# Kernel optimization log

Measured on AMD Instinct MI355X. Metric: run time of the kernel, lower is better.

Reference implementation:

```python
import jax, jax.numpy as jnp
import numpy as np

D_MODEL = 1024
N_HEADS = 16
D_HEAD = D_MODEL // N_HEADS
ROPE_BASE = 10000.0


def setup_inputs() -> dict:
    key = jax.random.key(0)
    k1, k2, k3, k4, k5 = jax.random.split(key, 5)
    std = 0.02 / np.sqrt(2 * 12)  # scaled_xavier with n_layers=12
    x = jax.random.normal(k1, (2, 2048, D_MODEL), dtype=jnp.float32)
    qkv_w = jax.random.normal(k2, (3 * D_MODEL, D_MODEL), dtype=jnp.float32) * std
    qkv_b = jnp.zeros((3 * D_MODEL,), dtype=jnp.float32)
    proj_w = jax.random.normal(k3, (D_MODEL, D_MODEL), dtype=jnp.float32) * std
    proj_b = jnp.zeros((D_MODEL,), dtype=jnp.float32)
    return {"x": x, "qkv_w": qkv_w, "qkv_b": qkv_b, "proj_w": proj_w, "proj_b": proj_b}


def _rope_cos_sin(seq_len, dtype):
    inv_freq = 1.0 / (ROPE_BASE ** (jnp.arange(0, D_HEAD, 2, dtype=jnp.float32) / D_HEAD))
    t = jnp.arange(seq_len, dtype=jnp.float32)
    freqs = jnp.einsum("t,d->td", t, inv_freq)          # [S, Dh/2]
    freqs = jnp.concatenate([freqs, freqs], axis=-1)      # [S, Dh]
    return jnp.cos(freqs).astype(dtype), jnp.sin(freqs).astype(dtype)


def _rotate_half(x):
    x1, x2 = jnp.split(x, 2, axis=-1)
    return jnp.concatenate([-x2, x1], axis=-1)


def reference(x, qkv_w, qkv_b, proj_w, proj_b):
    B, S, D = x.shape
    H, Dh = N_HEADS, D_HEAD
    scale = 1.0 / np.sqrt(Dh)

    qkv = x @ qkv_w.T + qkv_b                              # [B, S, 3D]
    qkv = qkv.reshape(B, S, 3, H, Dh)
    q = jnp.transpose(qkv[:, :, 0], (0, 2, 1, 3))          # [B, H, S, Dh]
    k = jnp.transpose(qkv[:, :, 1], (0, 2, 1, 3))
    v = jnp.transpose(qkv[:, :, 2], (0, 2, 1, 3))

    cos, sin = _rope_cos_sin(S, x.dtype)                   # [S, Dh]
    q = q * cos + _rotate_half(q) * sin
    k = k * cos + _rotate_half(k) * sin

    scores = jnp.einsum("bhsd,bhtd->bhst", q, k) * scale   # [B, H, S, S]
    causal = jnp.triu(jnp.ones((S, S), dtype=bool), k=1)
    neg = jnp.finfo(scores.dtype).min
    scores = jnp.where(causal[None, None], neg, scores)

    probs = jax.nn.softmax(scores, axis=-1)
    ctx = jnp.einsum("bhst,bhtd->bhsd", probs, v)          # [B, H, S, Dh]
    out = jnp.transpose(ctx, (0, 2, 1, 3)).reshape(B, S, D)
    out = out @ proj_w.T + proj_b
    return out
```

## Files before the change

kernel.cpp:

```cpp
#include <hip/hip_runtime.h>
#include <hip/hip_bf16.h>

#define BATCH 2
#define SEQ   2048
#define DMODEL 1024
#define NHEADS 16
#define DHEAD  64
#define MTOT   (BATCH * SEQ)
#define QKSTR  2048

typedef __attribute__((ext_vector_type(8))) short bf16x8;
typedef __attribute__((ext_vector_type(4))) short bf16x4;
typedef __attribute__((ext_vector_type(4))) float f32x4;

__device__ __forceinline__ void glds16(const void* g, void* l)
{
    __builtin_amdgcn_global_load_lds(
        (const __attribute__((address_space(1))) unsigned int*)g,
        (__attribute__((address_space(3))) unsigned int*)l, 16, 0, 0);
}

__device__ __forceinline__ unsigned cvt_pk_bf16(float lo, float hi)
{
    unsigned r;
    asm("v_cvt_pk_bf16_f32 %0, %1, %2" : "=v"(r) : "v"(lo), "v"(hi));
    return r;
}

__global__ void cast_all_kernel(
    const float* __restrict__ a, __hip_bfloat16* __restrict__ oa, int na4,
    const float* __restrict__ b, __hip_bfloat16* __restrict__ ob, int nb4,
    const float* __restrict__ c, __hip_bfloat16* __restrict__ oc, int nc4)
{
    int i = blockIdx.x * blockDim.x + threadIdx.x;
    const float* src; __hip_bfloat16* dst; int j = i;
    if (j < na4) { src = a; dst = oa; }
    else {
        j -= na4;
        if (j < nb4) { src = b; dst = ob; }
        else {
            j -= nb4;
            if (j >= nc4) return;
            src = c; dst = oc;
        }
    }
    float4 v = ((const float4*)src)[j];
    __hip_bfloat16 tmp[4];
    tmp[0] = __float2bfloat16(v.x);
    tmp[1] = __float2bfloat16(v.y);
    tmp[2] = __float2bfloat16(v.z);
    tmp[3] = __float2bfloat16(v.w);
    *(uint2*)(dst + 4 * (size_t)j) = *(const uint2*)tmp;
}

#define GBK 64

__device__ __forceinline__ void store_out(float* p, float v) { *p = v; }
__device__ __forceinline__ void store_out(__hip_bfloat16* p, float v) { *p = __float2bfloat16(v); }

template <typename OutT, int MODE, int TM, int TN, int MINW>
__global__ __launch_bounds__(256, MINW) void gemm_bias_kernel(
    const __hip_bfloat16* __restrict__ A, const __hip_bfloat16* __restrict__ W,
    const float* __restrict__ bias, OutT* __restrict__ out,
    __hip_bfloat16* __restrict__ vtg,
    int M, int N, int K)
{
    const int MI = TM / 32;
    const int NI = TN / 32;
    const int bm = blockIdx.x * TM;
    const int bn = blockIdx.y * TN;
    const int tid = threadIdx.x;
    const int wave = tid >> 6;
    const int lane = tid & 63;
    const int quad = lane >> 4;
    const int l16 = lane & 15;
    const int wm = (wave & 1) * (TM / 2);
    const int wn = (wave >> 1) * (TN / 2);

    __shared__ __hip_bfloat16 As[TM * GBK];
    __shared__ __hip_bfloat16 Bs[TN * GBK];

    f32x4 acc[MI][NI] = {};

    const int srow = lane >> 3;
    const int gc8 = (((lane & 7) ^ srow)) * 8;

    for (int kt = 0; kt < K; kt += GBK) {
#pragma unroll
        for (int t = 0; t < MI; t++) {
            int i = wave * MI + t;
            glds16(A + (size_t)(bm + i * 8 + srow) * K + kt + gc8, As + i * 512);
        }
#pragma unroll
        for (int t = 0; t < NI; t++) {
            int i = wave * NI + t;
            glds16(W + (size_t)(bn + i * 8 + srow) * K + kt + gc8, Bs + i * 512);
        }
        __syncthreads();

#pragma unroll
        for (int kk = 0; kk < 2; kk++) {
            bf16x8 af[MI], bfr[NI];
#pragma unroll
            for (int i = 0; i < MI; i++) {
                int ra = wm + i * 16 + l16;
                af[i] = *(const bf16x8*)(As + ra * 64 + (((kk << 2) + quad) ^ (ra & 7)) * 8);
            }
#pragma unroll
            for (int i = 0; i < NI; i++) {
                int rb = wn + i * 16 + l16;
                bfr[i] = *(const bf16x8*)(Bs + rb * 64 + (((kk << 2) + quad) ^ (rb & 7)) * 8);
            }
#pragma unroll
            for (int mi = 0; mi < MI; mi++)
#pragma unroll
                for (int ni = 0; ni < NI; ni++)
                    acc[mi][ni] = __builtin_amdgcn_mfma_f32_16x16x32_bf16(
                        af[mi], bfr[ni], acc[mi][ni], 0, 0, 0);
        }
        __syncthreads();
    }

    if (MODE == 1 && (bn + wn) < 2 * DMODEL) {
#pragma unroll
        for (int ni = 0; ni < 2; ni++) {
            int col = bn + wn + ni * 16 + l16;
            int i32 = col & 31;
            float invf = exp2f(-13.287712379549449f * (float)i32 * (1.0f / 32.0f));
            float b1 = bias[col], b2 = bias[col + 32];
#pragma unroll
            for (int mi = 0; mi < MI; mi++) {
#pragma unroll
                for (int r = 0; r < 4; r++) {
                    int row = bm + wm + mi * 16 + quad * 4 + r;
                    int s = row & (SEQ - 1);
                    float ang = (float)s * invf;
                    float sn, cs;
                    __sincosf(ang, &sn, &cs);
                    float x1 = acc[mi][ni][r] + b1;
                    float x2 = acc[mi][ni + 2][r] + b2;
                    store_out(&out[(size_t)row * QKSTR + col], x1 * cs - x2 * sn);
                    store_out(&out[(size_t)row * QKSTR + col + 32], x2 * cs + x1 * sn);
                }
            }
        }
    } else if (MODE == 1) {
#pragma unroll
        for (int ni = 0; ni < NI; ni++) {
            int colg = bn + wn + ni * 16 + l16;
            int vcol = colg - 2 * DMODEL;
            int hh = vcol >> 6, dh = vcol & 63;
            float bv = bias[colg];
#pragma unroll
            for (int mi = 0; mi < MI; mi++) {
                int row0 = bm + wm + mi * 16 + quad * 4;
                int bb = row0 >> 11;
                int ss = row0 & (SEQ - 1);
                __hip_bfloat16 tmp[4];
#pragma unroll
                for (int r = 0; r < 4; r++)
                    tmp[r] = __float2bfloat16(acc[mi][ni][r] + bv);
                *(uint2*)(vtg + (((size_t)bb * NHEADS + hh) * DHEAD + dh) * SEQ + ss) =
                    *(uint2*)tmp;
            }
        }
    } else {
#pragma unroll
        for (int mi = 0; mi < MI; mi++)
#pragma unroll
            for (int ni = 0; ni < NI; ni++) {
                int col = bn + wn + ni * 16 + l16;
                float bv = bias[col];
#pragma unroll
                for (int r = 0; r < 4; r++) {
                    int row = bm + wm + mi * 16 + quad * 4 + r;
                    store_out(&out[(size_t)row * N + col], acc[mi][ni][r] + bv);
                }
            }
    }
}

__global__ __launch_bounds__(256, 5) void flash_attn_mfma_kernel(
    const __hip_bfloat16* __restrict__ qkb,
    const __hip_bfloat16* __restrict__ vtg,
    __hip_bfloat16* __restrict__ ctx)
{
    const int bh = blockIdx.x;
    const int b = bh >> 4, h = bh & 15;
    const int y = blockIdx.y;
    const int qt = (y < 8) ? 31 - y : (y < 16) ? y - 8 : (y < 24) ? 39 - y : y - 16;
    const int tid = threadIdx.x;
    const int w = tid >> 6;
    const int lane = tid & 63;
    const int quad = lane >> 4;
    const int l16 = lane & 15;

    __shared__ alignas(16) __hip_bfloat16 Ks[2][64 * 64];
    __shared__ alignas(16) __hip_bfloat16 Vt[2][64 * 64];

    const __hip_bfloat16* qbase = qkb + (size_t)b * SEQ * QKSTR + h * DHEAD;
    const __hip_bfloat16* kbase = qbase + DMODEL;
    const __hip_bfloat16* vbase = vtg + (size_t)bh * DHEAD * SEQ;

    const __hip_bfloat16* qrow = qbase + (size_t)(qt * 64 + w * 16 + l16) * QKSTR;
    bf16x8 qf0 = *(const bf16x8*)(qrow + quad * 8);
    bf16x8 qf1 = *(const bf16x8*)(qrow + 32 + quad * 8);

    const int srow = lane >> 3;
    const int gc8 = ((lane & 7) ^ srow) * 8;
    const __hip_bfloat16* kg = kbase + (size_t)(w * 16 + srow) * QKSTR + gc8;
    const __hip_bfloat16* vg = vbase + (size_t)(w * 16 + srow) * SEQ + gc8;

    const int xr = l16 & 7;
    const int fo0 = l16 * 64 + ((quad ^ xr) << 3);
    const int fo1 = l16 * 64 + (((4 + quad) ^ xr) << 3);
    int vbse[4], vchk[4];
#pragma unroll
    for (int dt = 0; dt < 4; dt++)
        vbse[dt] = (dt * 16 + l16) * 64 + (quad & 1) * 4;
#pragma unroll
    for (int nt = 0; nt < 4; nt++)
        vchk[nt] = (((nt << 1) + (quad >> 1)) ^ xr) << 3;

    const short ov = (l16 == 0) ? (short)0x3F80 : (short)0;
    const bf16x4 ones4 = {ov, ov, ov, ov};

    f32x4 oacc[5] = {};

    auto stage = [&](int t, int buf) {
        const __hip_bfloat16* kt_ = kg + (size_t)t * 64 * QKSTR;
        const __hip_bfloat16* vt_ = vg + t * 64;
        glds16(kt_,              &Ks[buf][w * 1024]);
        glds16(kt_ + 8 * QKSTR,  &Ks[buf][w * 1024 + 512]);
        glds16(vt_,              &Vt[buf][w * 1024]);
        glds16(vt_ + 8 * SEQ,    &Vt[buf][w * 1024 + 512]);
    };

    stage(0, 0);

    for (int jt = 0; jt <= qt; jt++) {
        __syncthreads();
        const int cur = jt & 1;
        if (jt < qt) stage(jt + 1, cur ^ 1);
        const __hip_bfloat16* ks = Ks[cur];
        const __hip_bfloat16* vs = Vt[cur];

        f32x4 s4[4] = {};
        __builtin_amdgcn_s_setprio(1);
#pragma unroll
        for (int nt = 0; nt < 4; nt++)
            s4[nt] = __builtin_amdgcn_mfma_f32_16x16x32_bf16(
                *(const bf16x8*)(ks + nt * 1024 + fo0), qf0, s4[nt], 0, 0, 0);
#pragma unroll
        for (int nt = 0; nt < 4; nt++)
            s4[nt] = __builtin_amdgcn_mfma_f32_16x16x32_bf16(
                *(const bf16x8*)(ks + nt * 1024 + fo1), qf1, s4[nt], 0, 0, 0);
        __builtin_amdgcn_s_setprio(0);

        const bool diag = (jt == qt);
        const int qq = w * 16 + l16;
#pragma unroll
        for (int nt = 0; nt < 4; nt++) {
            float p0 = exp2f(s4[nt][0] * 0.1803368801f);
            float p1 = exp2f(s4[nt][1] * 0.1803368801f);
            float p2 = exp2f(s4[nt][2] * 0.1803368801f);
            float p3 = exp2f(s4[nt][3] * 0.1803368801f);
            if (diag) {
                int k0 = nt * 16 + quad * 4;
                p0 = (k0 + 0 <= qq) ? p0 : 0.f;
                p1 = (k0 + 1 <= qq) ? p1 : 0.f;
                p2 = (k0 + 2 <= qq) ? p2 : 0.f;
                p3 = (k0 + 3 <= qq) ? p3 : 0.f;
            }
            union { unsigned u[2]; bf16x4 v; } pu;
            pu.u[0] = cvt_pk_bf16(p0, p1);
            pu.u[1] = cvt_pk_bf16(p2, p3);
            const bf16x4 pa = pu.v;

            __builtin_amdgcn_s_setprio(1);
#pragma unroll
            for (int dt = 0; dt < 4; dt++)
                oacc[dt] = __builtin_amdgcn_mfma_f32_16x16x16bf16_1k(
                    pa, *(const bf16x4*)(vs + vbse[dt] + vchk[nt]), oacc[dt], 0, 0, 0);
            oacc[4] = __builtin_amdgcn_mfma_f32_16x16x16bf16_1k(
                pa, ones4, oacc[4], 0, 0, 0);
            __builtin_amdgcn_s_setprio(0);
        }
    }

#pragma unroll
    for (int r = 0; r < 4; r++) {
        float lv = __shfl(oacc[4][r], lane & 48);
        float il = 1.0f / lv;
        int qg = qt * 64 + w * 16 + quad * 4 + r;
        __hip_bfloat16* op = ctx + (((size_t)b * SEQ + qg) * NHEADS + h) * DHEAD + l16;
#pragma unroll
        for (int dt = 0; dt < 4; dt++)
            op[dt * 16] = __float2bfloat16(oacc[dt][r] * il);
    }
}

extern "C" void kernel_launch(void* const* d_in, const int* in_sizes, int n_in,
                              void* d_out, int out_size, void* d_ws, size_t ws_size,
                              hipStream_t stream)
{
    const float* x      = (const float*)d_in[0];
    const float* qkv_w  = (const float*)d_in[1];
    const float* qkv_b  = (const float*)d_in[2];
    const float* proj_w = (const float*)d_in[3];
    const float* proj_b = (const float*)d_in[4];
    float* out = (float*)d_out;

    char* w = (char*)d_ws;
    __hip_bfloat16* qkb = (__hip_bfloat16*)w;  w += (size_t)MTOT * QKSTR * 2;
    __hip_bfloat16* vtg = (__hip_bfloat16*)w;  w += (size_t)MTOT * DMODEL * 2;
    __hip_bfloat16* ctx = (__hip_bfloat16*)w;  w += (size_t)MTOT * DMODEL * 2;
    __hip_bfloat16* xb  = (__hip_bfloat16*)w;  w += (size_t)MTOT * DMODEL * 2;
    __hip_bfloat16* wqk = (__hip_bfloat16*)w;  w += (size_t)3 * DMODEL * DMODEL * 2;
    __hip_bfloat16* wpr = (__hip_bfloat16*)w;

    const int na4 = MTOT * DMODEL / 4;
    const int nb4 = 3 * DMODEL * DMODEL / 4;
    const int nc4 = DMODEL * DMODEL / 4;

    cast_all_kernel<<<(na4 + nb4 + nc4 + 255) / 256, 256, 0, stream>>>(
        x, xb, na4, qkv_w, wqk, nb4, proj_w, wpr, nc4);

    gemm_bias_kernel<__hip_bfloat16, 1, 128, 128, 3>
        <<<dim3(MTOT / 128, (3 * DMODEL) / 128), 256, 0, stream>>>(
        xb, wqk, qkv_b, qkb, vtg, MTOT, 3 * DMODEL, DMODEL);

    flash_attn_mfma_kernel<<<dim3(BATCH * NHEADS, 32), 256, 0, stream>>>(qkb, vtg, ctx);

    gemm_bias_kernel<float, 0, 64, 128, 6>
        <<<dim3(MTOT / 64, DMODEL / 128), 256, 0, stream>>>(
        ctx, wpr, proj_b, out, nullptr, MTOT, DMODEL, DMODEL);
}
```

Baseline: 174.1 us.

## Split attention KV tile across waves with triple-buffered loads and LDS reduction

Each wave now owns a 16-key slice of every KV tile and computes all 64 query rows against it. Its partial O and row-sum accumulators are reduced across waves through shared memory at the end. This cuts per-wave LDS reads of K and V, and the pipeline moves from double to triple buffering with explicit vmcnt waits in place of full syncthreads. exp2f becomes raw v_exp_f32, and the qt ordering is simplified to descending. The cost is a 4x larger accumulator register footprint (launch bounds drop from 5 to 3) and a cross-wave reduction epilogue.

```diff
diff --git a/kernel.cpp b/kernel.cpp
--- a/kernel.cpp
+++ b/kernel.cpp
@@ -24,6 +24,13 @@
 {
     unsigned r;
     asm("v_cvt_pk_bf16_f32 %0, %1, %2" : "=v"(r) : "v"(lo), "v"(hi));
+    return r;
+}
+
+__device__ __forceinline__ float fast_exp2(float x)
+{
+    float r;
+    asm("v_exp_f32 %0, %1" : "=v"(r) : "v"(x));
     return r;
 }
 
@@ -180,31 +187,36 @@
     }
 }
 
-__global__ __launch_bounds__(256, 5) void flash_attn_mfma_kernel(
+__global__ __launch_bounds__(256, 3) void flash_attn_mfma_kernel(
     const __hip_bfloat16* __restrict__ qkb,
     const __hip_bfloat16* __restrict__ vtg,
     __hip_bfloat16* __restrict__ ctx)
 {
     const int bh = blockIdx.x;
     const int b = bh >> 4, h = bh & 15;
-    const int y = blockIdx.y;
-    const int qt = (y < 8) ? 31 - y : (y < 16) ? y - 8 : (y < 24) ? 39 - y : y - 16;
+    const int qt = 31 - blockIdx.y;
     const int tid = threadIdx.x;
     const int w = tid >> 6;
     const int lane = tid & 63;
     const int quad = lane >> 4;
     const int l16 = lane & 15;
 
-    __shared__ alignas(16) __hip_bfloat16 Ks[2][64 * 64];
-    __shared__ alignas(16) __hip_bfloat16 Vt[2][64 * 64];
+    __shared__ alignas(16) __hip_bfloat16 smem[24576];
+    __hip_bfloat16* const ksb = smem;
+    __hip_bfloat16* const vtb = smem + 12288;
 
     const __hip_bfloat16* qbase = qkb + (size_t)b * SEQ * QKSTR + h * DHEAD;
     const __hip_bfloat16* kbase = qbase + DMODEL;
     const __hip_bfloat16* vbase = vtg + (size_t)bh * DHEAD * SEQ;
 
-    const __hip_bfloat16* qrow = qbase + (size_t)(qt * 64 + w * 16 + l16) * QKSTR;
-    bf16x8 qf0 = *(const bf16x8*)(qrow + quad * 8);
-    bf16x8 qf1 = *(const bf16x8*)(qrow + 32 + quad * 8);
+    bf16x8 qf[4][2];
+#pragma unroll
+    for (int tq = 0; tq < 4; tq++) {
+        const __hip_bfloat16* qr =
+            qbase + (size_t)(qt * 64 + tq * 16 + l16) * QKSTR;
+        qf[tq][0] = *(const bf16x8*)(qr + quad * 8);
+        qf[tq][1] = *(const bf16x8*)(qr + 32 + quad * 8);
+    }
 
     const int srow = lane >> 3;
     const int gc8 = ((lane & 7) ^ srow) * 8;
@@ -212,61 +224,71 @@
     const __hip_bfloat16* vg = vbase + (size_t)(w * 16 + srow) * SEQ + gc8;
 
     const int xr = l16 & 7;
-    const int fo0 = l16 * 64 + ((quad ^ xr) << 3);
-    const int fo1 = l16 * 64 + (((4 + quad) ^ xr) << 3);
-    int vbse[4], vchk[4];
+    const int foK0 = (w * 16 + l16) * 64 + ((quad ^ xr) << 3);
+    const int foK1 = (w * 16 + l16) * 64 + (((4 + quad) ^ xr) << 3);
+    int vb[4];
 #pragma unroll
     for (int dt = 0; dt < 4; dt++)
-        vbse[dt] = (dt * 16 + l16) * 64 + (quad & 1) * 4;
-#pragma unroll
-    for (int nt = 0; nt < 4; nt++)
-        vchk[nt] = (((nt << 1) + (quad >> 1)) ^ xr) << 3;
+        vb[dt] = (dt * 16 + l16) * 64 +
+                 ((((w << 1) + (quad >> 1)) ^ xr) << 3) + ((quad & 1) << 2);
 
     const short ov = (l16 == 0) ? (short)0x3F80 : (short)0;
     const bf16x4 ones4 = {ov, ov, ov, ov};
 
-    f32x4 oacc[5] = {};
+    f32x4 oacc[4][4] = {};
+    f32x4 lacc[4] = {};
 
     auto stage = [&](int t, int buf) {
         const __hip_bfloat16* kt_ = kg + (size_t)t * 64 * QKSTR;
         const __hip_bfloat16* vt_ = vg + t * 64;
-        glds16(kt_,              &Ks[buf][w * 1024]);
-        glds16(kt_ + 8 * QKSTR,  &Ks[buf][w * 1024 + 512]);
-        glds16(vt_,              &Vt[buf][w * 1024]);
-        glds16(vt_ + 8 * SEQ,    &Vt[buf][w * 1024 + 512]);
+        glds16(kt_,             ksb + buf * 4096 + w * 1024);
+        glds16(kt_ + 8 * QKSTR, ksb + buf * 4096 + w * 1024 + 512);
+        glds16(vt_,             vtb + buf * 4096 + w * 1024);
+        glds16(vt_ + 8 * SEQ,   vtb + buf * 4096 + w * 1024 + 512);
     };
 
     stage(0, 0);
-
+    stage(1, 1);
+
+    int cur = 0;
     for (int jt = 0; jt <= qt; jt++) {
-        __syncthreads();
-        const int cur = jt & 1;
-        if (jt < qt) stage(jt + 1, cur ^ 1);
-        const __hip_bfloat16* ks = Ks[cur];
-        const __hip_bfloat16* vs = Vt[cur];
-
+        if (jt < qt) asm volatile("s_waitcnt vmcnt(4)" ::: "memory");
+        else         asm volatile("s_waitcnt vmcnt(0)" ::: "memory");
+        __builtin_amdgcn_s_barrier();
+        __builtin_amdgcn_sched_barrier(0);
+
+        if (jt + 2 <= qt) {
+            int nb = cur + 2; if (nb >= 3) nb -= 3;
+            stage(jt + 2, nb);
+        }
+        const __hip_bfloat16* ks = ksb + cur * 4096;
+        const __hip_bfloat16* vs = vtb + cur * 4096;
+
+        bf16x8 ka0 = *(const bf16x8*)(ks + foK0);
+        bf16x8 ka1 = *(const bf16x8*)(ks + foK1);
         f32x4 s4[4] = {};
         __builtin_amdgcn_s_setprio(1);
 #pragma unroll
-        for (int nt = 0; nt < 4; nt++)
-            s4[nt] = __builtin_amdgcn_mfma_f32_16x16x32_bf16(
-                *(const bf16x8*)(ks + nt * 1024 + fo0), qf0, s4[nt], 0, 0, 0);
-#pragma unroll
-        for (int nt = 0; nt < 4; nt++)
-            s4[nt] = __builtin_amdgcn_mfma_f32_16x16x32_bf16(
-                *(const bf16x8*)(ks + nt * 1024 + fo1), qf1, s4[nt], 0, 0, 0);
+        for (int tq = 0; tq < 4; tq++)
+            s4[tq] = __builtin_amdgcn_mfma_f32_16x16x32_bf16(
+                ka0, qf[tq][0], s4[tq], 0, 0, 0);
+#pragma unroll
+        for (int tq = 0; tq < 4; tq++)
+            s4[tq] = __builtin_amdgcn_mfma_f32_16x16x32_bf16(
+                ka1, qf[tq][1], s4[tq], 0, 0, 0);
         __builtin_amdgcn_s_setprio(0);
 
         const bool diag = (jt == qt);
-        const int qq = w * 16 + l16;
-#pragma unroll
-        for (int nt = 0; nt < 4; nt++) {
-            float p0 = exp2f(s4[nt][0] * 0.1803368801f);
-            float p1 = exp2f(s4[nt][1] * 0.1803368801f);
-            float p2 = exp2f(s4[nt][2] * 0.1803368801f);
-            float p3 = exp2f(s4[nt][3] * 0.1803368801f);
+        bf16x4 pa[4];
+#pragma unroll
+        for (int tq = 0; tq < 4; tq++) {
+            float p0 = fast_exp2(s4[tq][0] * 0.1803368801f);
+            float p1 = fast_exp2(s4[tq][1] * 0.1803368801f);
+            float p2 = fast_exp2(s4[tq][2] * 0.1803368801f);
+            float p3 = fast_exp2(s4[tq][3] * 0.1803368801f);
             if (diag) {
-                int k0 = nt * 16 + quad * 4;
+                int k0 = w * 16 + quad * 4;
+                int qq = tq * 16 + l16;
                 p0 = (k0 + 0 <= qq) ? p0 : 0.f;
                 p1 = (k0 + 1 <= qq) ? p1 : 0.f;
                 p2 = (k0 + 2 <= qq) ? p2 : 0.f;
@@ -275,28 +297,73 @@
             union { unsigned u[2]; bf16x4 v; } pu;
             pu.u[0] = cvt_pk_bf16(p0, p1);
             pu.u[1] = cvt_pk_bf16(p2, p3);
-            const bf16x4 pa = pu.v;
-
-            __builtin_amdgcn_s_setprio(1);
-#pragma unroll
-            for (int dt = 0; dt < 4; dt++)
-                oacc[dt] = __builtin_amdgcn_mfma_f32_16x16x16bf16_1k(
-                    pa, *(const bf16x4*)(vs + vbse[dt] + vchk[nt]), oacc[dt], 0, 0, 0);
-            oacc[4] = __builtin_amdgcn_mfma_f32_16x16x16bf16_1k(
-                pa, ones4, oacc[4], 0, 0, 0);
-            __builtin_amdgcn_s_setprio(0);
-        }
-    }
-
-#pragma unroll
-    for (int r = 0; r < 4; r++) {
-        float lv = __shfl(oacc[4][r], lane & 48);
-        float il = 1.0f / lv;
-        int qg = qt * 64 + w * 16 + quad * 4 + r;
-        __hip_bfloat16* op = ctx + (((size_t)b * SEQ + qg) * NHEADS + h) * DHEAD + l16;
-#pragma unroll
-        for (int dt = 0; dt < 4; dt++)
-            op[dt * 16] = __float2bfloat16(oacc[dt][r] * il);
+            pa[tq] = pu.v;
+        }
+
+        bf16x4 vf0 = *(const bf16x4*)(vs + vb[0]);
+        bf16x4 vf1 = *(const bf16x4*)(vs + vb[1]);
+        bf16x4 vf2 = *(const bf16x4*)(vs + vb[2]);
+        bf16x4 vf3 = *(const bf16x4*)(vs + vb[3]);
+        __builtin_amdgcn_s_setprio(1);
+#pragma unroll
+        for (int tq = 0; tq < 4; tq++) {
+            oacc[tq][0] = __builtin_amdgcn_mfma_f32_16x16x16bf16_1k(
+                pa[tq], vf0, oacc[tq][0], 0, 0, 0);
+            oacc[tq][1] = __builtin_amdgcn_mfma_f32_16x16x16bf16_1k(
+                pa[tq], vf1, oacc[tq][1], 0, 0, 0);
+            oacc[tq][2] = __builtin_amdgcn_mfma_f32_16x16x16bf16_1k(
+                pa[tq], vf2, oacc[tq][2], 0, 0, 0);
+            oacc[tq][3] = __builtin_amdgcn_mfma_f32_16x16x16bf16_1k(
+                pa[tq], vf3, oacc[tq][3], 0, 0, 0);
+            lacc[tq] = __builtin_amdgcn_mfma_f32_16x16x16bf16_1k(
+                pa[tq], ones4, lacc[tq], 0, 0, 0);
+        }
+        __builtin_amdgcn_s_setprio(0);
+
+        cur = cur + 1; if (cur >= 3) cur -= 3;
+    }
+
+    __syncthreads();
+    f32x4* const osh = (f32x4*)smem;
+    f32x4* const lsh = (f32x4*)(smem + 16384);
+
+    if (l16 == 0) {
+#pragma unroll
+        for (int tq = 0; tq < 4; tq++)
+            lsh[(w * 4 + tq) * 4 + quad] = lacc[tq];
+    }
+    __syncthreads();
+    f32x4 lt = lsh[(0 * 4 + w) * 4 + quad];
+#pragma unroll
+    for (int src = 1; src < 4; src++)
+        lt += lsh[(src * 4 + w) * 4 + quad];
+    f32x4 ilv;
+#pragma unroll
+    for (int r = 0; r < 4; r++) ilv[r] = 1.0f / lt[r];
+
+#pragma unroll
+    for (int p = 0; p < 2; p++) {
+        if (p) __syncthreads();
+#pragma unroll
+        for (int tq = 0; tq < 4; tq++)
+#pragma unroll
+            for (int d = 0; d < 2; d++)
+                osh[((w * 4 + tq) * 2 + d) * 64 + lane] = oacc[tq][p * 2 + d];
+        __syncthreads();
+#pragma unroll
+        for (int d = 0; d < 2; d++) {
+            f32x4 os = osh[((0 * 4 + w) * 2 + d) * 64 + lane];
+#pragma unroll
+            for (int src = 1; src < 4; src++)
+                os += osh[((src * 4 + w) * 2 + d) * 64 + lane];
+            const int dh = (p * 2 + d) * 16 + l16;
+#pragma unroll
+            for (int r = 0; r < 4; r++) {
+                int qg = qt * 64 + w * 16 + quad * 4 + r;
+                ctx[(((size_t)b * SEQ + qg) * NHEADS + h) * DHEAD + dh] =
+                    __float2bfloat16(os[r] * ilv[r]);
+            }
+        }
     }
 }
 
```

Measured after the change: 166.8 us. 1.04x faster.
